# Performance work log

Measured on AMD Instinct MI355X. Metric: run time of the kernel, lower is better.

Reference implementation:

```python
import jax, jax.numpy as jnp
import numpy as np

C = 256
HEADS = 4
ATT = C // HEADS
GROUPS = 32
EPS = 1e-6


def group_norm(x, gamma, beta):
    # x: [b, c, h, w]
    b, c, h, w = x.shape
    xg = x.reshape(b, GROUPS, c // GROUPS, h, w)
    mu = jnp.mean(xg, axis=(2, 3, 4), keepdims=True)
    var = jnp.var(xg, axis=(2, 3, 4), keepdims=True)
    xg = (xg - mu) * jax.lax.rsqrt(var + EPS)
    x = xg.reshape(b, c, h, w)
    return x * gamma[None, :, None, None] + beta[None, :, None, None]


def conv1x1(x, w, b):
    # w: [c_out, c_in], x: [b, c_in, h, w]
    return jnp.einsum('oc,bchw->bohw', w, x) + b[None, :, None, None]


def setup_inputs() -> dict:
    key = jax.random.key(0)
    ks = jax.random.split(key, 8)
    b, h, w = 2, 64, 64
    x = jax.random.normal(ks[0], (b, C, h, w), dtype=jnp.float32)
    y = jax.random.normal(ks[1], (b, C, h, w), dtype=jnp.float32)
    s = 1.0 / np.sqrt(C)
    return {
        'x': x,
        'y': y,
        'g1': jnp.ones((C,), jnp.float32),
        'b1': jnp.zeros((C,), jnp.float32),
        'g2': jnp.ones((C,), jnp.float32),
        'b2': jnp.zeros((C,), jnp.float32),
        'wq': jax.random.normal(ks[2], (C, C), jnp.float32) * s,
        'bq': jnp.zeros((C,), jnp.float32),
        'wk': jax.random.normal(ks[3], (C, C), jnp.float32) * s,
        'bk': jnp.zeros((C,), jnp.float32),
        'wv': jax.random.normal(ks[4], (C, C), jnp.float32) * s,
        'bv': jnp.zeros((C,), jnp.float32),
        'wo': jax.random.normal(ks[5], (C, C), jnp.float32) * s,
        'bo': jnp.zeros((C,), jnp.float32),
    }


def reference(x, y, g1, b1, g2, b2, wq, bq, wk, bk, wv, bv, wo, bo):
    b, c, h, w = x.shape
    s = h * w
    h_ = group_norm(x, g1, b1)
    yn = group_norm(y, g2, b2)
    q = conv1x1(yn, wq, bq)
    k = conv1x1(h_, wk, bk)
    v = conv1x1(h_, wv, bv)
    # [b, c, h, w] -> [b, heads, att, s] -> [b, heads, s, att]
    def split_heads(t):
        return t.reshape(b, HEADS, ATT, s).transpose(0, 1, 3, 2)
    q = split_heads(q) * (ATT ** -0.5)
    k = split_heads(k)
    v = split_heads(v)
    scores = jnp.einsum('bnsd,bntd->bnst', q, k)        # [b, heads, s, s]
    attn = jax.nn.softmax(scores, axis=-1)
    out = jnp.einsum('bnst,bntd->bnsd', attn, v)        # [b, heads, s, att]
    # [b, heads, s, att] -> [b, s, heads, att] -> [b, h, w, c] -> [b, c, h, w]
    out = out.transpose(0, 2, 1, 3).reshape(b, h, w, c).transpose(0, 3, 1, 2)
    out = conv1x1(out, wo, bo)
    return x + out
```

## Files before the change

kernel.cpp:

```cpp
#include <hip/hip_runtime.h>

typedef __bf16 bf16_t;
typedef bf16_t bf16x8 __attribute__((ext_vector_type(8)));
typedef float f32x4 __attribute__((ext_vector_type(4)));

#define MFMA16(a,b,c) __builtin_amdgcn_mfma_f32_16x16x32_bf16((a),(b),(c),0,0,0)

#define GLOAD_LDS16(gsrc, ldst) \
  __builtin_amdgcn_global_load_lds((const __attribute__((address_space(1))) unsigned int*)(gsrc), \
                                   (__attribute__((address_space(3))) unsigned int*)(ldst), 16, 0, 0)

__device__ __forceinline__ unsigned short f2bf(float f){
  unsigned int u = __builtin_bit_cast(unsigned int, f);
  u = (u + 0x7FFFu + ((u >> 16) & 1u)) >> 16;
  return (unsigned short)u;
}
__device__ __forceinline__ float bf2f(unsigned short u){
  return __builtin_bit_cast(float, (unsigned int)u << 16);
}
__device__ __forceinline__ ushort4 pk4(f32x4 v){
  union { __bf16 b[4]; ushort4 u; } r;
  r.b[0]=(__bf16)v[0]; r.b[1]=(__bf16)v[1]; r.b[2]=(__bf16)v[2]; r.b[3]=(__bf16)v[3];
  return r.u;
}

__device__ __forceinline__ int KI(int d){
  int gi = (d >> 2) & 15;
  int pos = (gi & 8) | ((gi & 3) << 1) | ((gi >> 2) & 1);
  return (d & ~63) | (pos << 2);
}

__device__ __forceinline__ int BL256(int r, int c){
  return ((r >> 4) << 12) + (((c >> 5)) << 9) + ((r & 15) << 5)
       + (((c & 15) >> 2) << 3) + (((c >> 4) & 1) << 2) + (c & 3);
}

constexpr int BN = 2;
constexpr int CC = 256;
constexpr int S  = 4096;
constexpr int HH = 4;
constexpr int DD = 64;

constexpr size_t OFF_WQ = 0;
constexpr size_t OFF_WK = 65536;
constexpr size_t OFF_WV = 131072;
constexpr size_t OFF_WO = 196608;
constexpr size_t OFF_NY = 262144;
constexpr size_t OFF_NX = OFF_NY + (size_t)BN*S*CC;
constexpr size_t OFF_Q  = OFF_NX + (size_t)BN*S*CC;
constexpr size_t OFF_K  = OFF_Q  + (size_t)BN*S*CC;
constexpr size_t OFF_V  = OFF_K  + (size_t)BN*S*CC;
constexpr size_t OFF_AO = OFF_V  + (size_t)BN*S*CC;
__device__ __forceinline__ unsigned short* pacc_base(unsigned short* ws, int ch){
  return ws + (ch == 0 ? OFF_NY : (ch == 1 ? OFF_NX : OFF_AO));
}

__global__ __launch_bounds__(256) void prep_k(const float* __restrict__ x, const float* __restrict__ y,
    const float* __restrict__ g1, const float* __restrict__ b1,
    const float* __restrict__ g2, const float* __restrict__ b2,
    const float* __restrict__ wq, const float* __restrict__ wk,
    const float* __restrict__ wv, const float* __restrict__ wo,
    unsigned short* __restrict__ ws)
{
  __shared__ float red[8];
  __shared__ float mv[2];
  const int tid = threadIdx.x;
  const int bid = blockIdx.x;

  if (bid >= 128){
    const int idx = (bid - 128)*256 + tid;
    const int m = idx >> 14;
    const int off = (idx & 16383) << 2;
    const float* src = (m==0) ? wq : (m==1) ? wk : (m==2) ? wv : wo;
    float4 v = *(const float4*)(src + off);
    ushort4 r; r.x=f2bf(v.x); r.y=f2bf(v.y); r.z=f2bf(v.z); r.w=f2bf(v.w);
    const int o = off >> 8, c = off & 255;
    *(ushort4*)(ws + (size_t)m*65536 + BL256(o, c)) = r;
    return;
  }

  const int tsel = bid >> 6;
  const int rem  = bid & 63;
  const int b = rem >> 5, g = rem & 31;
  const float* in = (tsel ? y : x) + ((size_t)b*CC + g*8)*S;
  unsigned short* outp = ws + (tsel ? OFF_NY : OFF_NX) + (size_t)b*S*CC;
  const int j = g & 3;
  const int gk = (g >> 2) * 512;
  const int posA = (j & 1)*16 + (j >> 1)*4;
  const int posB = posA + 8;
  const float* gamma = (tsel ? g2 : g1) + g*8;
  const float* beta  = (tsel ? b2 : b1) + g*8;

  float s = 0.f, ss = 0.f;
  #pragma unroll
  for (int ci = 0; ci < 8; ci++){
    const float4* row = (const float4*)(in + (size_t)ci*S);
    #pragma unroll
    for (int i = 0; i < 4; i++){
      float4 v = row[tid + i*256];
      s  += v.x + v.y + v.z + v.w;
      ss += v.x*v.x + v.y*v.y + v.z*v.z + v.w*v.w;
    }
  }
  #pragma unroll
  for (int off = 1; off < 64; off <<= 1){
    s  += __shfl_xor(s,  off);
    ss += __shfl_xor(ss, off);
  }
  const int wave = tid >> 6, lane = tid & 63;
  if (lane == 0){ red[wave] = s; red[4+wave] = ss; }
  __syncthreads();
  if (tid == 0){
    float S1 = red[0]+red[1]+red[2]+red[3];
    float S2 = red[4]+red[5]+red[6]+red[7];
    const float invn = 1.0f/32768.0f;
    float mean = S1*invn;
    float var  = S2*invn - mean*mean;
    mv[0] = mean; mv[1] = rsqrtf(var + 1e-6f);
  }
  __syncthreads();
  const float mean = mv[0], rstd = mv[1];
  float sc[8], sh[8];
  #pragma unroll
  for (int ci = 0; ci < 8; ci++){ sc[ci] = rstd*gamma[ci]; sh[ci] = beta[ci] - mean*sc[ci]; }
  for (int i = 0; i < 16; i++){
    const int p = tid + i*256;
    const int base = ((p >> 4) << 12) + gk + ((p & 15) << 5);
    ushort4 a0, a1;
    a0.x = f2bf(in[0*S+p]*sc[0]+sh[0]);
    a0.y = f2bf(in[1*S+p]*sc[1]+sh[1]);
    a0.z = f2bf(in[2*S+p]*sc[2]+sh[2]);
    a0.w = f2bf(in[3*S+p]*sc[3]+sh[3]);
    a1.x = f2bf(in[4*S+p]*sc[4]+sh[4]);
    a1.y = f2bf(in[5*S+p]*sc[5]+sh[5]);
    a1.z = f2bf(in[6*S+p]*sc[6]+sh[6]);
    a1.w = f2bf(in[7*S+p]*sc[7]+sh[7]);
    *(ushort4*)(outp + base + posA) = a0;
    *(ushort4*)(outp + base + posB) = a1;
  }
}

__global__ __launch_bounds__(256, 3) void qkv_gemm(unsigned short* __restrict__ ws,
    const float* __restrict__ bq, const float* __restrict__ bk, const float* __restrict__ bv)
{
  const int tid = threadIdx.x;
  const int lane = tid & 63, wave = tid >> 6;
  const int lq = lane & 15, lg = lane >> 4;
  const int lofs = lq*32 + lg*8;
  const int bid = blockIdx.x;

  if (bid < 512){
    const int inst2 = bid >> 7;
    const int which = inst2 >> 1;
    const int b = inst2 & 1;
    const int tile = bid & 127;
    const int mtile = tile & 3;
    const int ntile = tile >> 2;
    const int mbase = mtile*64 + (wave>>1)*32;
    const int nbase = ntile*128 + (wave&1)*64;
    const unsigned short* Amat = ws + (which==0 ? OFF_WQ : OFF_WK);
    const unsigned short* Bmat = ws + (which==0 ? OFF_NY : OFF_NX) + (size_t)b*S*CC;

    f32x4 acc[2][4];
    #pragma unroll
    for (int i = 0; i < 2; i++)
      #pragma unroll
      for (int j = 0; j < 4; j++)
        acc[i][j] = (f32x4){0.f,0.f,0.f,0.f};

    const unsigned short* Arow = Amat + (size_t)mbase*CC + lofs;
    const unsigned short* Brow = Bmat + (size_t)nbase*CC + lofs;
    for (int ks = 0; ks < CC; ks += 32) {
      bf16x8 af[2], bfr[4];
      #pragma unroll
      for (int mt = 0; mt < 2; mt++)
        af[mt] = *(const bf16x8*)(Arow + mt*16*CC + ks*16);
      #pragma unroll
      for (int nt = 0; nt < 4; nt++)
        bfr[nt] = *(const bf16x8*)(Brow + nt*16*CC + ks*16);
      #pragma unroll
      for (int mt = 0; mt < 2; mt++)
        #pragma unroll
        for (int nt = 0; nt < 4; nt++)
          acc[mt][nt] = MFMA16(af[mt], bfr[nt], acc[mt][nt]);
    }

    const float* bias = (which==0) ? bq : bk;
    const float scl = (which==0) ? 0.125f*1.44269504089f : 1.0f;
    unsigned short* Outp = ws + (which==0 ? OFF_Q : OFF_K) + (size_t)b*HH*S*DD;
    #pragma unroll
    for (int mt = 0; mt < 2; mt++){
      const int o = mbase + mt*16 + lg*4;
      const float4 bb = *(const float4*)(bias + o);
      const int hd = o >> 6, db = KI(o & 63);
      #pragma unroll
      for (int nt = 0; nt < 4; nt++){
        const int p = nbase + nt*16 + lq;
        f32x4 v = acc[mt][nt];
        ushort4 r;
        r.x = f2bf((v[0]+bb.x)*scl); r.y = f2bf((v[1]+bb.y)*scl);
        r.z = f2bf((v[2]+bb.z)*scl); r.w = f2bf((v[3]+bb.w)*scl);
        *(ushort4*)(Outp + ((size_t)hd*S + p)*DD + db) = r;
      }
    }
  } else {
    const int r0 = bid - 512;
    const int b = r0 >> 7;
    const int tile = r0 & 127;
    const int mtile = tile >> 2;
    const int ntile = tile & 3;
    const int mbase = mtile*128 + (wave>>1)*64;
    const int nbase = ntile*64 + (wave&1)*32;
    const unsigned short* Amat = ws + OFF_NX + (size_t)b*S*CC;
    const unsigned short* Bmat = ws + OFF_WV;

    f32x4 acc[4][2];
    #pragma unroll
    for (int i = 0; i < 4; i++)
      #pragma unroll
      for (int j = 0; j < 2; j++)
        acc[i][j] = (f32x4){0.f,0.f,0.f,0.f};

    const unsigned short* Arow = Amat + (size_t)mbase*CC + lofs;
    const unsigned short* Brow = Bmat + (size_t)nbase*CC + lofs;
    for (int ks = 0; ks < CC; ks += 32) {
      bf16x8 af[4], bfr[2];
      #pragma unroll
      for (int mt = 0; mt < 4; mt++)
        af[mt] = *(const bf16x8*)(Arow + mt*16*CC + ks*16);
      #pragma unroll
      for (int nt = 0; nt < 2; nt++)
        bfr[nt] = *(const bf16x8*)(Brow + nt*16*CC + ks*16);
      #pragma unroll
      for (int mt = 0; mt < 4; mt++)
        #pragma unroll
        for (int nt = 0; nt < 2; nt++)
          acc[mt][nt] = MFMA16(af[mt], bfr[nt], acc[mt][nt]);
    }

    unsigned short* Outp = ws + OFF_V + (size_t)b*CC*S;
    #pragma unroll
    for (int nt = 0; nt < 2; nt++){
      const int o = nbase + nt*16 + lq;
      const float bb = bv[o];
      #pragma unroll
      for (int mt = 0; mt < 4; mt++){
        const int p = mbase + mt*16 + lg*4;
        f32x4 v = acc[mt][nt];
        ushort4 r;
        r.x = f2bf(v[0]+bb); r.y = f2bf(v[1]+bb);
        r.z = f2bf(v[2]+bb); r.w = f2bf(v[3]+bb);
        *(ushort4*)(Outp + (size_t)o*S + KI(p)) = r;
      }
    }
  }
}

__global__ __launch_bounds__(256, 3) void attn_k(unsigned short* __restrict__ ws)
{
  __shared__ __align__(1024) char lds[32768];
  const int tid = threadIdx.x;
  const int lane = tid & 63, wave = tid >> 6;
  const int lq = lane & 15, lg = lane >> 4;
  const int rsw = (lq & 7) << 4;
  const int bid = blockIdx.x;
  const int bh = bid & 7;
  const int rest = bid >> 3;
  const int qblk = rest & 31;
  const int ch = rest >> 5;
  const int tBeg = ch*1344 + (ch ? 64 : 0);
  const int tEnd = tBeg + 1344 + (ch ? 0 : 64);
  const unsigned short* Qp = ws + OFF_Q + (size_t)bh*S*DD;
  const unsigned short* Kp = ws + OFF_K + (size_t)bh*S*DD;
  const int b = bh >> 2, h = bh & 3;
  const unsigned short* Vp = ws + OFF_V + ((size_t)b*CC + h*DD)*S;
  const int qbw = qblk*128 + wave*32;

  bf16x8 qf[2][2];
  #pragma unroll
  for (int f = 0; f < 2; f++)
    #pragma unroll
    for (int hh = 0; hh < 2; hh++)
      qf[f][hh] = *(const bf16x8*)(Qp + (size_t)(qbw + f*16 + lq)*DD + hh*32 + lg*8);

  bf16x8 ones;
  #pragma unroll
  for (int i = 0; i < 8; i++) ones[i] = (__bf16)1.0f;

  const int csel = ((lane & 7) ^ ((lane >> 3) & 7)) * 8;
  const int srow = wave*16 + (lane >> 3);
  const int kofs0 = lq*128 + ((lg*16) ^ rsw);
  const int kofs1 = kofs0 ^ 64;

  f32x4 acc[4][2];
  #pragma unroll
  for (int i = 0; i < 4; i++)
    #pragma unroll
    for (int f = 0; f < 2; f++)
      acc[i][f] = (f32x4){0.f,0.f,0.f,0.f};
  f32x4 accL[2] = {(f32x4){0.f,0.f,0.f,0.f}, (f32x4){0.f,0.f,0.f,0.f}};
  float mr[2] = {-1e30f, -1e30f};

  #pragma unroll
  for (int j = 0; j < 2; j++){
    const int row = srow + j*8;
    GLOAD_LDS16(Kp + (size_t)(tBeg + row)*DD + csel, lds + wave*2048 + j*1024);
    GLOAD_LDS16(Vp + (size_t)row*S + tBeg + csel,    lds + 16384 + wave*2048 + j*1024);
  }
  __syncthreads();

  int cur = 0;
  for (int t0 = tBeg; t0 < tEnd; t0 += 64){
    const char* kb = lds + cur*8192;
    const char* vb = lds + 16384 + cur*8192;
    if (t0 + 64 < tEnd){
      char* kn = lds + (cur^1)*8192;
      char* vn = lds + 16384 + (cur^1)*8192;
      #pragma unroll
      for (int j = 0; j < 2; j++){
        const int row = srow + j*8;
        GLOAD_LDS16(Kp + (size_t)(t0 + 64 + row)*DD + csel, kn + wave*2048 + j*1024);
        GLOAD_LDS16(Vp + (size_t)row*S + (t0 + 64) + csel,  vn + wave*2048 + j*1024);
      }
    }
    bf16x8 kf[4][2];
    #pragma unroll
    for (int mt = 0; mt < 4; mt++){
      kf[mt][0] = *(const bf16x8*)(kb + mt*2048 + kofs0);
      kf[mt][1] = *(const bf16x8*)(kb + mt*2048 + kofs1);
    }
    f32x4 st[2][4];
    __builtin_amdgcn_s_setprio(1);
    #pragma unroll
    for (int f = 0; f < 2; f++)
      #pragma unroll
      for (int mt = 0; mt < 4; mt++){
        f32x4 z = (f32x4){0.f,0.f,0.f,0.f};
        z = MFMA16(kf[mt][0], qf[f][0], z);
        z = MFMA16(kf[mt][1], qf[f][1], z);
        st[f][mt] = z;
      }
    __builtin_amdgcn_s_setprio(0);
    bf16x8 vf[4][2];
    #pragma unroll
    for (int dt = 0; dt < 4; dt++){
      vf[dt][0] = *(const bf16x8*)(vb + dt*2048 + kofs0);
      vf[dt][1] = *(const bf16x8*)(vb + dt*2048 + kofs1);
    }
    float tmv[2];
    #pragma unroll
    for (int f = 0; f < 2; f++){
      float tm = fmaxf(
        fmaxf(fmaxf(fmaxf(st[f][0][0], st[f][0][1]), fmaxf(st[f][0][2], st[f][0][3])),
              fmaxf(fmaxf(st[f][1][0], st[f][1][1]), fmaxf(st[f][1][2], st[f][1][3]))),
        fmaxf(fmaxf(fmaxf(st[f][2][0], st[f][2][1]), fmaxf(st[f][2][2], st[f][2][3])),
              fmaxf(fmaxf(st[f][3][0], st[f][3][1]), fmaxf(st[f][3][2], st[f][3][3]))));
      tm = fmaxf(tm, __shfl_xor(tm, 16));
      tm = fmaxf(tm, __shfl_xor(tm, 32));
      tmv[f] = tm;
    }
    if (!__all((tmv[0] <= mr[0] + 8.f) && (tmv[1] <= mr[1] + 8.f))){
      #pragma unroll
      for (int f = 0; f < 2; f++){
        const float mnew = fmaxf(mr[f], tmv[f]);
        const float c = __builtin_amdgcn_exp2f(mr[f] - mnew);
        #pragma unroll
        for (int dt = 0; dt < 4; dt++)
          #pragma unroll
          for (int r = 0; r < 4; r++)
            acc[dt][f][r] *= c;
        #pragma unroll
        for (int r = 0; r < 4; r++) accL[f][r] *= c;
        mr[f] = mnew;
      }
    }
    union PU { bf16x8 v; __bf16 e[8]; } p0[2], p1[2];
    #pragma unroll
    for (int f = 0; f < 2; f++){
      #pragma unroll
      for (int mt = 0; mt < 4; mt++)
        #pragma unroll
        for (int r = 0; r < 4; r++){
          float e = __builtin_amdgcn_exp2f(st[f][mt][r] - mr[f]);
          if (mt < 2) p0[f].e[mt*4+r] = (__bf16)e;
          else        p1[f].e[(mt-2)*4+r] = (__bf16)e;
        }
    }
    __builtin_amdgcn_s_setprio(1);
    #pragma unroll
    for (int dt = 0; dt < 4; dt++)
      #pragma unroll
      for (int f = 0; f < 2; f++){
        f32x4 a = acc[dt][f];
        a = MFMA16(vf[dt][0], p0[f].v, a);
        a = MFMA16(vf[dt][1], p1[f].v, a);
        acc[dt][f] = a;
      }
    #pragma unroll
    for (int f = 0; f < 2; f++){
      accL[f] = MFMA16(ones, p0[f].v, accL[f]);
      accL[f] = MFMA16(ones, p1[f].v, accL[f]);
    }
    __builtin_amdgcn_s_setprio(0);
    __syncthreads();
    cur ^= 1;
  }

  unsigned short* PA = pacc_base(ws, ch) + (size_t)bh*S*DD;
  float* ML = (float*)(ws + OFF_Q) + ((size_t)ch*8 + bh)*S*2;
  #pragma unroll
  for (int f = 0; f < 2; f++){
    const int q = qbw + f*16 + lq;
    #pragma unroll
    for (int dt = 0; dt < 4; dt++)
      *(ushort4*)(PA + (size_t)q*DD + dt*16 + lg*4) = pk4(acc[dt][f]);
    if (lg == 0){
      ML[(size_t)q*2]   = mr[f];
      ML[(size_t)q*2+1] = accL[f][0];
    }
  }
}

__global__ __launch_bounds__(256, 2) void outproj_k(unsigned short* __restrict__ ws,
    const float* __restrict__ bo, const float* __restrict__ x, float* __restrict__ out)
{
  __shared__ unsigned short ldsA[16384];
  __shared__ float wtab[64][4][3];
  const int tid = threadIdx.x;
  const int lane = tid & 63, wave = tid >> 6;
  const int lq = lane & 15, lg = lane >> 4;
  const int lofs = lq*32 + lg*8;
  const int bid = blockIdx.x;
  const int b = bid >> 8;
  const int r0 = bid & 255;
  const int mtile = r0 >> 2;
  const int ntile = r0 & 3;
  const int qg = mtile*64;

  {
    const int q = tid >> 2, h = tid & 3;
    const float* MLb = (const float*)(ws + OFF_Q);
    float m[3], l[3];
    #pragma unroll
    for (int c = 0; c < 3; c++){
      const float* p = MLb + (((size_t)c*8 + b*4 + h)*S + (qg + q))*2;
      m[c] = p[0]; l[c] = p[1];
    }
    const float M = fmaxf(m[0], fmaxf(m[1], m[2]));
    const float w0 = __builtin_amdgcn_exp2f(m[0] - M);
    const float w1 = __builtin_amdgcn_exp2f(m[1] - M);
    const float w2 = __builtin_amdgcn_exp2f(m[2] - M);
    const float inv = 1.0f / (w0*l[0] + w1*l[1] + w2*l[2]);
    wtab[q][h][0] = w0*inv; wtab[q][h][1] = w1*inv; wtab[q][h][2] = w2*inv;
  }
  __syncthreads();

  #pragma unroll
  for (int it = 0; it < 16; it++){
    const int w = it*256 + tid;
    const int q = w >> 6, cq = w & 63;
    const int h = cq >> 4, d = (cq & 15)*4;
    const size_t po = ((size_t)(b*4 + h)*S + (qg + q))*DD + d;
    const ushort4 a0 = *(const ushort4*)(ws + OFF_NY + po);
    const ushort4 a1 = *(const ushort4*)(ws + OFF_NX + po);
    const ushort4 a2 = *(const ushort4*)(ws + OFF_AO + po);
    const float w0 = wtab[q][h][0], w1 = wtab[q][h][1], w2 = wtab[q][h][2];
    f32x4 v;
    v[0] = bf2f(a0.x)*w0 + bf2f(a1.x)*w1 + bf2f(a2.x)*w2;
    v[1] = bf2f(a0.y)*w0 + bf2f(a1.y)*w1 + bf2f(a2.y)*w2;
    v[2] = bf2f(a0.z)*w0 + bf2f(a1.z)*w1 + bf2f(a2.z)*w2;
    v[3] = bf2f(a0.w)*w0 + bf2f(a1.w)*w1 + bf2f(a2.w)*w2;
    *(ushort4*)(ldsA + BL256(q, cq*4)) = pk4(v);
  }
  __syncthreads();

  const int mbase = (wave>>1)*32;
  const int nbase = ntile*64 + (wave&1)*32;
  f32x4 acc[2][2];
  #pragma unroll
  for (int i = 0; i < 2; i++)
    #pragma unroll
    for (int j = 0; j < 2; j++)
      acc[i][j] = (f32x4){0.f,0.f,0.f,0.f};
  const unsigned short* Arow = ldsA + (size_t)mbase*CC + lofs;
  const unsigned short* Brow = ws + OFF_WO + (size_t)nbase*CC + lofs;
  for (int ks = 0; ks < CC; ks += 32) {
    bf16x8 af[2], bfr[2];
    #pragma unroll
    for (int mt = 0; mt < 2; mt++)
      af[mt] = *(const bf16x8*)(Arow + mt*16*CC + ks*16);
    #pragma unroll
    for (int nt = 0; nt < 2; nt++)
      bfr[nt] = *(const bf16x8*)(Brow + nt*16*CC + ks*16);
    #pragma unroll
    for (int mt = 0; mt < 2; mt++)
      #pragma unroll
      for (int nt = 0; nt < 2; nt++)
        acc[mt][nt] = MFMA16(af[mt], bfr[nt], acc[mt][nt]);
  }
  #pragma unroll
  for (int nt = 0; nt < 2; nt++){
    const int o = nbase + nt*16 + lq;
    const float bb = bo[o];
    #pragma unroll
    for (int mt = 0; mt < 2; mt++){
      const int p = qg + mbase + mt*16 + lg*4;
      const size_t idx = ((size_t)b*CC + o)*S + p;
      const float4 xr = *(const float4*)(x + idx);
      f32x4 v = acc[mt][nt];
      float4 r; r.x = v[0]+bb+xr.x; r.y = v[1]+bb+xr.y; r.z = v[2]+bb+xr.z; r.w = v[3]+bb+xr.w;
      *(float4*)(out + idx) = r;
    }
  }
}

extern "C" void kernel_launch(void* const* d_in, const int* in_sizes, int n_in,
                              void* d_out, int out_size, void* d_ws, size_t ws_size,
                              hipStream_t stream) {
  const float* x  = (const float*)d_in[0];
  const float* y  = (const float*)d_in[1];
  const float* g1 = (const float*)d_in[2];
  const float* b1 = (const float*)d_in[3];
  const float* g2 = (const float*)d_in[4];
  const float* b2 = (const float*)d_in[5];
  const float* wq = (const float*)d_in[6];
  const float* bq = (const float*)d_in[7];
  const float* wk = (const float*)d_in[8];
  const float* bk = (const float*)d_in[9];
  const float* wv = (const float*)d_in[10];
  const float* bv = (const float*)d_in[11];
  const float* wo = (const float*)d_in[12];
  const float* bo = (const float*)d_in[13];
  float* out = (float*)d_out;
  unsigned short* ws16 = (unsigned short*)d_ws;

  prep_k   <<<384, 256, 0, stream>>>(x, y, g1, b1, g2, b2, wq, wk, wv, wo, ws16);
  qkv_gemm <<<768, 256, 0, stream>>>(ws16, bq, bk, bv);
  attn_k   <<<768, 256, 0, stream>>>(ws16);
  outproj_k<<<512, 256, 0, stream>>>(ws16, bo, x, out);
}
```

Baseline: 108.5 us.

## Fuse output projection into attention kernel via last-arriving-block counter

Removes the separate outproj kernel. Each attention block increments a per-(batch, query-block) atomic counter, and the twelfth block to arrive merges the three split partial results and runs the Wo GEMM plus residual for 128 queries. Also swaps manual bf16 rounding for v_cvt_pk_bf16_f32 and uses v_max3 for the row max. It moves the cross-lane max shuffles into the rare rescale branch and drops the s_setprio hints. This saves a kernel launch and the inter-kernel gap, but the projection now runs on only 64 blocks at the tail, which can serialize work.

```diff
diff --git a/kernel.cpp b/kernel.cpp
--- a/kernel.cpp
+++ b/kernel.cpp
@@ -10,18 +10,19 @@
   __builtin_amdgcn_global_load_lds((const __attribute__((address_space(1))) unsigned int*)(gsrc), \
                                    (__attribute__((address_space(3))) unsigned int*)(ldst), 16, 0, 0)
 
-__device__ __forceinline__ unsigned short f2bf(float f){
-  unsigned int u = __builtin_bit_cast(unsigned int, f);
-  u = (u + 0x7FFFu + ((u >> 16) & 1u)) >> 16;
-  return (unsigned short)u;
+__device__ __forceinline__ unsigned cvtpk(float lo, float hi){
+  unsigned r; asm("v_cvt_pk_bf16_f32 %0, %1, %2" : "=v"(r) : "v"(lo), "v"(hi)); return r;
+}
+__device__ __forceinline__ ushort4 pk4f(float a, float b, float c, float d){
+  union { unsigned u[2]; ushort4 s; } r;
+  r.u[0] = cvtpk(a, b); r.u[1] = cvtpk(c, d); return r.s;
+}
+__device__ __forceinline__ ushort4 pk4(f32x4 v){ return pk4f(v[0], v[1], v[2], v[3]); }
+__device__ __forceinline__ float max3f(float a, float b, float c){
+  float r; asm("v_max3_f32 %0, %1, %2, %3" : "=v"(r) : "v"(a), "v"(b), "v"(c)); return r;
 }
 __device__ __forceinline__ float bf2f(unsigned short u){
   return __builtin_bit_cast(float, (unsigned int)u << 16);
-}
-__device__ __forceinline__ ushort4 pk4(f32x4 v){
-  union { __bf16 b[4]; ushort4 u; } r;
-  r.b[0]=(__bf16)v[0]; r.b[1]=(__bf16)v[1]; r.b[2]=(__bf16)v[2]; r.b[3]=(__bf16)v[3];
-  return r.u;
 }
 
 __device__ __forceinline__ int KI(int d){
@@ -51,6 +52,7 @@
 constexpr size_t OFF_K  = OFF_Q  + (size_t)BN*S*CC;
 constexpr size_t OFF_V  = OFF_K  + (size_t)BN*S*CC;
 constexpr size_t OFF_AO = OFF_V  + (size_t)BN*S*CC;
+constexpr size_t WS_NEED_BYTES = (OFF_AO + (size_t)BN*S*CC) * 2;
 __device__ __forceinline__ unsigned short* pacc_base(unsigned short* ws, int ch){
   return ws + (ch == 0 ? OFF_NY : (ch == 1 ? OFF_NX : OFF_AO));
 }
@@ -73,9 +75,8 @@
     const int off = (idx & 16383) << 2;
     const float* src = (m==0) ? wq : (m==1) ? wk : (m==2) ? wv : wo;
     float4 v = *(const float4*)(src + off);
-    ushort4 r; r.x=f2bf(v.x); r.y=f2bf(v.y); r.z=f2bf(v.z); r.w=f2bf(v.w);
     const int o = off >> 8, c = off & 255;
-    *(ushort4*)(ws + (size_t)m*65536 + BL256(o, c)) = r;
+    *(ushort4*)(ws + (size_t)m*65536 + BL256(o, c)) = pk4f(v.x, v.y, v.z, v.w);
     return;
   }
 
@@ -126,15 +127,10 @@
   for (int i = 0; i < 16; i++){
     const int p = tid + i*256;
     const int base = ((p >> 4) << 12) + gk + ((p & 15) << 5);
-    ushort4 a0, a1;
-    a0.x = f2bf(in[0*S+p]*sc[0]+sh[0]);
-    a0.y = f2bf(in[1*S+p]*sc[1]+sh[1]);
-    a0.z = f2bf(in[2*S+p]*sc[2]+sh[2]);
-    a0.w = f2bf(in[3*S+p]*sc[3]+sh[3]);
-    a1.x = f2bf(in[4*S+p]*sc[4]+sh[4]);
-    a1.y = f2bf(in[5*S+p]*sc[5]+sh[5]);
-    a1.z = f2bf(in[6*S+p]*sc[6]+sh[6]);
-    a1.w = f2bf(in[7*S+p]*sc[7]+sh[7]);
+    ushort4 a0 = pk4f(in[0*S+p]*sc[0]+sh[0], in[1*S+p]*sc[1]+sh[1],
+                      in[2*S+p]*sc[2]+sh[2], in[3*S+p]*sc[3]+sh[3]);
+    ushort4 a1 = pk4f(in[4*S+p]*sc[4]+sh[4], in[5*S+p]*sc[5]+sh[5],
+                      in[6*S+p]*sc[6]+sh[6], in[7*S+p]*sc[7]+sh[7]);
     *(ushort4*)(outp + base + posA) = a0;
     *(ushort4*)(outp + base + posB) = a1;
   }
@@ -197,10 +193,8 @@
       for (int nt = 0; nt < 4; nt++){
         const int p = nbase + nt*16 + lq;
         f32x4 v = acc[mt][nt];
-        ushort4 r;
-        r.x = f2bf((v[0]+bb.x)*scl); r.y = f2bf((v[1]+bb.y)*scl);
-        r.z = f2bf((v[2]+bb.z)*scl); r.w = f2bf((v[3]+bb.w)*scl);
-        *(ushort4*)(Outp + ((size_t)hd*S + p)*DD + db) = r;
+        *(ushort4*)(Outp + ((size_t)hd*S + p)*DD + db) =
+          pk4f((v[0]+bb.x)*scl, (v[1]+bb.y)*scl, (v[2]+bb.z)*scl, (v[3]+bb.w)*scl);
       }
     }
   } else {
@@ -247,18 +241,19 @@
       for (int mt = 0; mt < 4; mt++){
         const int p = mbase + mt*16 + lg*4;
         f32x4 v = acc[mt][nt];
-        ushort4 r;
-        r.x = f2bf(v[0]+bb); r.y = f2bf(v[1]+bb);
-        r.z = f2bf(v[2]+bb); r.w = f2bf(v[3]+bb);
-        *(ushort4*)(Outp + (size_t)o*S + KI(p)) = r;
-      }
-    }
-  }
-}
-
-__global__ __launch_bounds__(256, 3) void attn_k(unsigned short* __restrict__ ws)
+        *(ushort4*)(Outp + (size_t)o*S + KI(p)) = pk4f(v[0]+bb, v[1]+bb, v[2]+bb, v[3]+bb);
+      }
+    }
+  }
+}
+
+__global__ __launch_bounds__(256, 3) void attn_k(unsigned short* __restrict__ ws,
+    const float* __restrict__ bo, const float* __restrict__ x, float* __restrict__ out,
+    unsigned int* __restrict__ ctr)
 {
   __shared__ __align__(1024) char lds[32768];
+  __shared__ float wtab[128][4][3];
+  __shared__ int winflag;
   const int tid = threadIdx.x;
   const int lane = tid & 63, wave = tid >> 6;
   const int lq = lane & 15, lg = lane >> 4;
@@ -330,7 +325,6 @@
       kf[mt][1] = *(const bf16x8*)(kb + mt*2048 + kofs1);
     }
     f32x4 st[2][4];
-    __builtin_amdgcn_s_setprio(1);
     #pragma unroll
     for (int f = 0; f < 2; f++)
       #pragma unroll
@@ -340,7 +334,6 @@
         z = MFMA16(kf[mt][1], qf[f][1], z);
         st[f][mt] = z;
       }
-    __builtin_amdgcn_s_setprio(0);
     bf16x8 vf[4][2];
     #pragma unroll
     for (int dt = 0; dt < 4; dt++){
@@ -350,19 +343,19 @@
     float tmv[2];
     #pragma unroll
     for (int f = 0; f < 2; f++){
-      float tm = fmaxf(
-        fmaxf(fmaxf(fmaxf(st[f][0][0], st[f][0][1]), fmaxf(st[f][0][2], st[f][0][3])),
-              fmaxf(fmaxf(st[f][1][0], st[f][1][1]), fmaxf(st[f][1][2], st[f][1][3]))),
-        fmaxf(fmaxf(fmaxf(st[f][2][0], st[f][2][1]), fmaxf(st[f][2][2], st[f][2][3])),
-              fmaxf(fmaxf(st[f][3][0], st[f][3][1]), fmaxf(st[f][3][2], st[f][3][3]))));
-      tm = fmaxf(tm, __shfl_xor(tm, 16));
-      tm = fmaxf(tm, __shfl_xor(tm, 32));
-      tmv[f] = tm;
+      float a0 = max3f(st[f][0][0], st[f][0][1], st[f][0][2]);
+      float a1 = max3f(st[f][0][3], st[f][1][0], st[f][1][1]);
+      float a2 = max3f(st[f][1][2], st[f][1][3], st[f][2][0]);
+      float a3 = max3f(st[f][2][1], st[f][2][2], st[f][2][3]);
+      float a4 = max3f(st[f][3][0], st[f][3][1], st[f][3][2]);
+      tmv[f] = fmaxf(max3f(a0, a1, st[f][3][3]), fmaxf(a2, max3f(a3, a4, -1e30f)));
     }
     if (!__all((tmv[0] <= mr[0] + 8.f) && (tmv[1] <= mr[1] + 8.f))){
       #pragma unroll
       for (int f = 0; f < 2; f++){
-        const float mnew = fmaxf(mr[f], tmv[f]);
+        float tx = fmaxf(tmv[f], __shfl_xor(tmv[f], 16));
+        tx = fmaxf(tx, __shfl_xor(tx, 32));
+        const float mnew = fmaxf(mr[f], tx);
         const float c = __builtin_amdgcn_exp2f(mr[f] - mnew);
         #pragma unroll
         for (int dt = 0; dt < 4; dt++)
@@ -374,19 +367,19 @@
         mr[f] = mnew;
       }
     }
-    union PU { bf16x8 v; __bf16 e[8]; } p0[2], p1[2];
+    union PU { bf16x8 v; unsigned u[4]; } p0[2], p1[2];
     #pragma unroll
     for (int f = 0; f < 2; f++){
       #pragma unroll
-      for (int mt = 0; mt < 4; mt++)
-        #pragma unroll
-        for (int r = 0; r < 4; r++){
-          float e = __builtin_amdgcn_exp2f(st[f][mt][r] - mr[f]);
-          if (mt < 2) p0[f].e[mt*4+r] = (__bf16)e;
-          else        p1[f].e[(mt-2)*4+r] = (__bf16)e;
-        }
-    }
-    __builtin_amdgcn_s_setprio(1);
+      for (int mt = 0; mt < 4; mt++){
+        float e0 = __builtin_amdgcn_exp2f(st[f][mt][0] - mr[f]);
+        float e1 = __builtin_amdgcn_exp2f(st[f][mt][1] - mr[f]);
+        float e2 = __builtin_amdgcn_exp2f(st[f][mt][2] - mr[f]);
+        float e3 = __builtin_amdgcn_exp2f(st[f][mt][3] - mr[f]);
+        if (mt < 2){ p0[f].u[mt*2] = cvtpk(e0, e1); p0[f].u[mt*2+1] = cvtpk(e2, e3); }
+        else       { p1[f].u[(mt-2)*2] = cvtpk(e0, e1); p1[f].u[(mt-2)*2+1] = cvtpk(e2, e3); }
+      }
+    }
     #pragma unroll
     for (int dt = 0; dt < 4; dt++)
       #pragma unroll
@@ -401,7 +394,6 @@
       accL[f] = MFMA16(ones, p0[f].v, accL[f]);
       accL[f] = MFMA16(ones, p1[f].v, accL[f]);
     }
-    __builtin_amdgcn_s_setprio(0);
     __syncthreads();
     cur ^= 1;
   }
@@ -419,98 +411,104 @@
       ML[(size_t)q*2+1] = accL[f][0];
     }
   }
-}
-
-__global__ __launch_bounds__(256, 2) void outproj_k(unsigned short* __restrict__ ws,
-    const float* __restrict__ bo, const float* __restrict__ x, float* __restrict__ out)
-{
-  __shared__ unsigned short ldsA[16384];
-  __shared__ float wtab[64][4][3];
-  const int tid = threadIdx.x;
-  const int lane = tid & 63, wave = tid >> 6;
-  const int lq = lane & 15, lg = lane >> 4;
+
+  __threadfence();
+  __syncthreads();
+  if (tid == 0){
+    unsigned old = atomicAdd(&ctr[b*32 + qblk], 1u);
+    winflag = ((old % 12u) == 11u);
+  }
+  __syncthreads();
+  if (!winflag) return;
+  __threadfence();
+
+  const float* MLb = (const float*)(ws + OFF_Q);
+  #pragma unroll
+  for (int it = 0; it < 2; it++){
+    const int idx = it*256 + tid;
+    const int ql = idx >> 2, hh = idx & 3;
+    const int q = qblk*128 + ql;
+    float m0, m1, m2, l0, l1, l2;
+    {
+      const float* p0p = MLb + (((size_t)0*8 + b*4 + hh)*S + q)*2;
+      const float* p1p = MLb + (((size_t)1*8 + b*4 + hh)*S + q)*2;
+      const float* p2p = MLb + (((size_t)2*8 + b*4 + hh)*S + q)*2;
+      m0 = p0p[0]; l0 = p0p[1];
+      m1 = p1p[0]; l1 = p1p[1];
+      m2 = p2p[0]; l2 = p2p[1];
+    }
+    const float M = max3f(m0, m1, m2);
+    const float w0 = __builtin_amdgcn_exp2f(m0 - M);
+    const float w1 = __builtin_amdgcn_exp2f(m1 - M);
+    const float w2 = __builtin_amdgcn_exp2f(m2 - M);
+    const float inv = 1.0f / (w0*l0 + w1*l1 + w2*l2);
+    wtab[ql][hh][0] = w0*inv; wtab[ql][hh][1] = w1*inv; wtab[ql][hh][2] = w2*inv;
+  }
+  __syncthreads();
+
   const int lofs = lq*32 + lg*8;
-  const int bid = blockIdx.x;
-  const int b = bid >> 8;
-  const int r0 = bid & 255;
-  const int mtile = r0 >> 2;
-  const int ntile = r0 & 3;
-  const int qg = mtile*64;
-
-  {
-    const int q = tid >> 2, h = tid & 3;
-    const float* MLb = (const float*)(ws + OFF_Q);
-    float m[3], l[3];
-    #pragma unroll
-    for (int c = 0; c < 3; c++){
-      const float* p = MLb + (((size_t)c*8 + b*4 + h)*S + (qg + q))*2;
-      m[c] = p[0]; l[c] = p[1];
-    }
-    const float M = fmaxf(m[0], fmaxf(m[1], m[2]));
-    const float w0 = __builtin_amdgcn_exp2f(m[0] - M);
-    const float w1 = __builtin_amdgcn_exp2f(m[1] - M);
-    const float w2 = __builtin_amdgcn_exp2f(m[2] - M);
-    const float inv = 1.0f / (w0*l[0] + w1*l[1] + w2*l[2]);
-    wtab[q][h][0] = w0*inv; wtab[q][h][1] = w1*inv; wtab[q][h][2] = w2*inv;
-  }
-  __syncthreads();
-
-  #pragma unroll
-  for (int it = 0; it < 16; it++){
-    const int w = it*256 + tid;
-    const int q = w >> 6, cq = w & 63;
-    const int h = cq >> 4, d = (cq & 15)*4;
-    const size_t po = ((size_t)(b*4 + h)*S + (qg + q))*DD + d;
-    const ushort4 a0 = *(const ushort4*)(ws + OFF_NY + po);
-    const ushort4 a1 = *(const ushort4*)(ws + OFF_NX + po);
-    const ushort4 a2 = *(const ushort4*)(ws + OFF_AO + po);
-    const float w0 = wtab[q][h][0], w1 = wtab[q][h][1], w2 = wtab[q][h][2];
-    f32x4 v;
-    v[0] = bf2f(a0.x)*w0 + bf2f(a1.x)*w1 + bf2f(a2.x)*w2;
-    v[1] = bf2f(a0.y)*w0 + bf2f(a1.y)*w1 + bf2f(a2.y)*w2;
-    v[2] = bf2f(a0.z)*w0 + bf2f(a1.z)*w1 + bf2f(a2.z)*w2;
-    v[3] = bf2f(a0.w)*w0 + bf2f(a1.w)*w1 + bf2f(a2.w)*w2;
-    *(ushort4*)(ldsA + BL256(q, cq*4)) = pk4(v);
-  }
-  __syncthreads();
-
-  const int mbase = (wave>>1)*32;
-  const int nbase = ntile*64 + (wave&1)*32;
-  f32x4 acc[2][2];
-  #pragma unroll
-  for (int i = 0; i < 2; i++)
-    #pragma unroll
-    for (int j = 0; j < 2; j++)
-      acc[i][j] = (f32x4){0.f,0.f,0.f,0.f};
-  const unsigned short* Arow = ldsA + (size_t)mbase*CC + lofs;
-  const unsigned short* Brow = ws + OFF_WO + (size_t)nbase*CC + lofs;
-  for (int ks = 0; ks < CC; ks += 32) {
-    bf16x8 af[2], bfr[2];
-    #pragma unroll
-    for (int mt = 0; mt < 2; mt++)
-      af[mt] = *(const bf16x8*)(Arow + mt*16*CC + ks*16);
-    #pragma unroll
-    for (int nt = 0; nt < 2; nt++)
-      bfr[nt] = *(const bf16x8*)(Brow + nt*16*CC + ks*16);
-    #pragma unroll
-    for (int mt = 0; mt < 2; mt++)
-      #pragma unroll
-      for (int nt = 0; nt < 2; nt++)
-        acc[mt][nt] = MFMA16(af[mt], bfr[nt], acc[mt][nt]);
-  }
-  #pragma unroll
-  for (int nt = 0; nt < 2; nt++){
-    const int o = nbase + nt*16 + lq;
-    const float bb = bo[o];
-    #pragma unroll
-    for (int mt = 0; mt < 2; mt++){
-      const int p = qg + mbase + mt*16 + lg*4;
-      const size_t idx = ((size_t)b*CC + o)*S + p;
-      const float4 xr = *(const float4*)(x + idx);
-      f32x4 v = acc[mt][nt];
-      float4 r; r.x = v[0]+bb+xr.x; r.y = v[1]+bb+xr.y; r.z = v[2]+bb+xr.z; r.w = v[3]+bb+xr.w;
-      *(float4*)(out + idx) = r;
-    }
+  unsigned short* ldsA = (unsigned short*)lds;
+  #pragma unroll
+  for (int qh = 0; qh < 2; qh++){
+    const int qg = qblk*128 + qh*64;
+    #pragma unroll
+    for (int it = 0; it < 16; it++){
+      const int w = it*256 + tid;
+      const int ql = w >> 6, cq = w & 63;
+      const int hh = cq >> 4, d = (cq & 15)*4;
+      const size_t po = ((size_t)(b*4 + hh)*S + qg + ql)*DD + d;
+      const ushort4 a0 = *(const ushort4*)(ws + OFF_NY + po);
+      const ushort4 a1 = *(const ushort4*)(ws + OFF_NX + po);
+      const ushort4 a2 = *(const ushort4*)(ws + OFF_AO + po);
+      const float w0 = wtab[qh*64 + ql][hh][0];
+      const float w1 = wtab[qh*64 + ql][hh][1];
+      const float w2 = wtab[qh*64 + ql][hh][2];
+      *(ushort4*)(ldsA + BL256(ql, cq*4)) = pk4f(
+        bf2f(a0.x)*w0 + bf2f(a1.x)*w1 + bf2f(a2.x)*w2,
+        bf2f(a0.y)*w0 + bf2f(a1.y)*w1 + bf2f(a2.y)*w2,
+        bf2f(a0.z)*w0 + bf2f(a1.z)*w1 + bf2f(a2.z)*w2,
+        bf2f(a0.w)*w0 + bf2f(a1.w)*w1 + bf2f(a2.w)*w2);
+    }
+    __syncthreads();
+    const int mb = (wave >> 1)*32;
+    const int nb = (wave & 1)*128;
+    f32x4 acc2[2][8];
+    #pragma unroll
+    for (int i = 0; i < 2; i++)
+      #pragma unroll
+      for (int j = 0; j < 8; j++)
+        acc2[i][j] = (f32x4){0.f,0.f,0.f,0.f};
+    const unsigned short* Arow = ldsA + (size_t)mb*CC + lofs;
+    const unsigned short* Brow = ws + OFF_WO + (size_t)nb*CC + lofs;
+    for (int ks = 0; ks < CC; ks += 32){
+      bf16x8 af[2], bfr[8];
+      #pragma unroll
+      for (int mt = 0; mt < 2; mt++)
+        af[mt] = *(const bf16x8*)(Arow + mt*16*CC + ks*16);
+      #pragma unroll
+      for (int nt = 0; nt < 8; nt++)
+        bfr[nt] = *(const bf16x8*)(Brow + nt*16*CC + ks*16);
+      #pragma unroll
+      for (int mt = 0; mt < 2; mt++)
+        #pragma unroll
+        for (int nt = 0; nt < 8; nt++)
+          acc2[mt][nt] = MFMA16(af[mt], bfr[nt], acc2[mt][nt]);
+    }
+    #pragma unroll
+    for (int nt = 0; nt < 8; nt++){
+      const int o = nb + nt*16 + lq;
+      const float bb = bo[o];
+      #pragma unroll
+      for (int mt = 0; mt < 2; mt++){
+        const int p = qg + mb + mt*16 + lg*4;
+        const size_t idx = ((size_t)b*CC + o)*S + p;
+        const float4 xr = *(const float4*)(x + idx);
+        f32x4 v = acc2[mt][nt];
+        float4 r; r.x = v[0]+bb+xr.x; r.y = v[1]+bb+xr.y; r.z = v[2]+bb+xr.z; r.w = v[3]+bb+xr.w;
+        *(float4*)(out + idx) = r;
+      }
+    }
+    __syncthreads();
   }
 }
 
@@ -534,8 +532,15 @@
   float* out = (float*)d_out;
   unsigned short* ws16 = (unsigned short*)d_ws;
 
-  prep_k   <<<384, 256, 0, stream>>>(x, y, g1, b1, g2, b2, wq, wk, wv, wo, ws16);
-  qkv_gemm <<<768, 256, 0, stream>>>(ws16, bq, bk, bv);
-  attn_k   <<<768, 256, 0, stream>>>(ws16);
-  outproj_k<<<512, 256, 0, stream>>>(ws16, bo, x, out);
-}
+  unsigned int* ctr;
+  if (ws_size >= WS_NEED_BYTES + 256){
+    ctr = (unsigned int*)((char*)d_ws + WS_NEED_BYTES);
+    hipMemsetAsync(ctr, 0, 256, stream);
+  } else {
+    ctr = (unsigned int*)(ws16 + OFF_WQ);
+  }
+
+  prep_k  <<<384, 256, 0, stream>>>(x, y, g1, b1, g2, b2, wq, wk, wv, wo, ws16);
+  qkv_gemm<<<768, 256, 0, stream>>>(ws16, bq, bk, bv);
+  attn_k  <<<768, 256, 0, stream>>>(ws16, bo, x, out, ctr);
+}
```

Result: slower. 195.0 us (+79.6%).
